# Kernel optimization log

Hardware: AMD Instinct MI355X
Metric: run time of the kernel (lower is better)

The kernel has to match this reference:

```python
import jax, jax.numpy as jnp
import numpy as np

N_NODES = 50000
N_REL = 20
EMB = 64
HID = 128
N_EDGES = 1600000
BATCH = 8192


def _rgcn_layer(x, src, dst, etype, W, root, b):
    # PyG RGCNConv with aggr='mean', no basis decomposition:
    # out[i] = sum_r W_r @ mean_{j in N_r(i)} x[j] + root @ x[i] + b
    # Mean commutes with the linear map, so aggregate x[src] per (dst, rel)
    # first, then apply W_r once per relation.
    n, r = N_NODES, N_REL
    seg = dst * r + etype                                   # [E]
    msg = x[src]                                            # [E, d_in]
    agg = jax.ops.segment_sum(msg, seg, num_segments=n * r)  # [N*R, d_in]
    cnt = jax.ops.segment_sum(jnp.ones(src.shape, x.dtype), seg, num_segments=n * r)
    mean = agg / jnp.maximum(cnt, 1.0)[:, None]
    mean = mean.reshape(n, r, -1)                           # [N, R, d_in]
    return jnp.einsum('nri,rio->no', mean, W) + x @ root + b


def setup_inputs() -> dict:
    key = jax.random.key(0)
    ks = jax.random.split(key, 16)
    edge_index = jax.random.randint(ks[0], (2, N_EDGES), 0, N_NODES, dtype=jnp.int64 if jax.config.jax_enable_x64 else jnp.int32)
    edge_type = jax.random.randint(ks[1], (N_EDGES,), 0, N_REL)
    head_indices = jax.random.randint(ks[2], (BATCH,), 0, N_NODES)
    tail_indices = jax.random.randint(ks[3], (BATCH,), 0, N_NODES)
    relation_types = jax.random.randint(ks[4], (BATCH,), 0, N_REL)

    def xavier(k, shape):
        fan_in, fan_out = shape[-2], shape[-1]
        lim = float(np.sqrt(6.0 / (fan_in + fan_out)))
        return jax.random.uniform(k, shape, jnp.float32, -lim, lim)

    node_emb = xavier(ks[5], (N_NODES, EMB))
    W1 = xavier(ks[6], (N_REL, EMB, HID))
    root1 = xavier(ks[7], (EMB, HID))
    b1 = jnp.zeros((HID,), jnp.float32)
    W2 = xavier(ks[8], (N_REL, HID, HID))
    root2 = xavier(ks[9], (HID, HID))
    b2 = jnp.zeros((HID,), jnp.float32)
    rel_emb = xavier(ks[10], (N_REL, HID))
    return dict(edge_index=edge_index, edge_type=edge_type,
                head_indices=head_indices, tail_indices=tail_indices,
                relation_types=relation_types, node_emb=node_emb,
                W1=W1, root1=root1, b1=b1, W2=W2, root2=root2, b2=b2,
                rel_emb=rel_emb)


def reference(edge_index, edge_type, head_indices, tail_indices, relation_types,
              node_emb, W1, root1, b1, W2, root2, b2, rel_emb):
    src, dst = edge_index[0], edge_index[1]
    # RGCN encoder (eval mode: dropout is identity)
    h = _rgcn_layer(node_emb, src, dst, edge_type, W1, root1, b1)
    h = jax.nn.relu(h)
    h = _rgcn_layer(h, src, dst, edge_type, W2, root2, b2)
    # DistMult decoder
    head = h[head_indices]
    tail = h[tail_indices]
    r = rel_emb[relation_types]
    scores = jnp.sum(head * r * tail, axis=1)               # [B]
    return scores
```

## Files before the change

### kernel.cpp

```cpp
#include <hip/hip_runtime.h>
#include <hip/hip_bf16.h>

#define NNODES 50000
#define NREL   20
#define NSEG   (NNODES * NREL)
#define DEMB   64
#define DHID   128

typedef __attribute__((ext_vector_type(8))) short short8;
typedef __attribute__((ext_vector_type(4))) float f32x4;

__device__ __forceinline__ unsigned short bf16rn(float x) {
    unsigned u = __builtin_bit_cast(unsigned, x);
    unsigned r = u + 0x7FFFu + ((u >> 16) & 1u);
    return (unsigned short)(r >> 16);
}
__device__ __forceinline__ float bf16tof(unsigned short h) {
    return __builtin_bit_cast(float, (unsigned)h << 16);
}


__global__ void hist_kernel(const int* __restrict__ dst, const int* __restrict__ et,
                            int E, int* __restrict__ cnt) {
    for (int e = blockIdx.x * blockDim.x + threadIdx.x; e < E; e += gridDim.x * blockDim.x) {
        atomicAdd(&cnt[dst[e] * NREL + et[e]], 1);
    }
}

__global__ void scan_partial(const int* __restrict__ cnt, int* __restrict__ bsum, int n) {
    __shared__ int s[256];
    int base = blockIdx.x * 1024;
    int t = threadIdx.x;
    int v = 0;
    for (int i = t; i < 1024; i += 256) {
        int idx = base + i;
        v += (idx < n) ? cnt[idx] : 0;
    }
    s[t] = v;
    __syncthreads();
    for (int o = 128; o > 0; o >>= 1) {
        if (t < o) s[t] += s[t + o];
        __syncthreads();
    }
    if (t == 0) bsum[blockIdx.x] = s[0];
}

__global__ void scan_bsums(int* __restrict__ bsum, int nb) {
    __shared__ int s[1024];
    int t = threadIdx.x;
    s[t] = (t < nb) ? bsum[t] : 0;
    __syncthreads();
    for (int o = 1; o < 1024; o <<= 1) {
        int v = (t >= o) ? s[t - o] : 0;
        __syncthreads();
        s[t] += v;
        __syncthreads();
    }
    if (t < nb) bsum[t] = (t == 0) ? 0 : s[t - 1];
}

__global__ void scan_final(const int* __restrict__ cnt, const int* __restrict__ bsum,
                           int* __restrict__ off, int n) {
    __shared__ int s[256];
    int base = blockIdx.x * 1024;
    int t = threadIdx.x;
    int idx = base + t * 4;
    int a0 = (idx + 0 < n) ? cnt[idx + 0] : 0;
    int a1 = (idx + 1 < n) ? cnt[idx + 1] : 0;
    int a2 = (idx + 2 < n) ? cnt[idx + 2] : 0;
    int a3 = (idx + 3 < n) ? cnt[idx + 3] : 0;
    s[t] = a0 + a1 + a2 + a3;
    __syncthreads();
    for (int o = 1; o < 256; o <<= 1) {
        int v = (t >= o) ? s[t - o] : 0;
        __syncthreads();
        s[t] += v;
        __syncthreads();
    }
    int base_ex = ((t == 0) ? 0 : s[t - 1]) + bsum[blockIdx.x];
    if (idx + 0 < n) off[idx + 0] = base_ex;
    if (idx + 1 < n) off[idx + 1] = base_ex + a0;
    if (idx + 2 < n) off[idx + 2] = base_ex + a0 + a1;
    if (idx + 3 < n) off[idx + 3] = base_ex + a0 + a1 + a2;
}

__global__ void place_kernel(const int* __restrict__ src, const int* __restrict__ dst,
                             const int* __restrict__ et, int E,
                             int* __restrict__ off_mut, int* __restrict__ csr_src) {
    for (int e = blockIdx.x * blockDim.x + threadIdx.x; e < E; e += gridDim.x * blockDim.x) {
        int seg = dst[e] * NREL + et[e];
        int p = atomicAdd(&off_mut[seg], 1);
        csr_src[p] = src[e];
    }
}

template <int K>
__global__ void prep_w(const float* __restrict__ W, const float* __restrict__ root,
                       short* __restrict__ Wt) {
    constexpr int KS = K / 32;
    int idx = blockIdx.x * blockDim.x + threadIdx.x;
    int total = (NREL + 1) * 128 * K;
    if (idx >= total) return;
    int r   = idx / (128 * K);
    int rem = idx % (128 * K);
    int c   = rem / K;
    int k   = rem % K;
    float v = (r < NREL) ? W[((size_t)r * K + k) * 128 + c] : root[(size_t)k * 128 + c];
    unsigned short hi = bf16rn(v);
    unsigned short lo = bf16rn(v - bf16tof(hi));
    int s = k >> 5, kk = k & 31;
    size_t base = ((size_t)r * KS + s) * 10240 + (size_t)c * 40 + kk;
    Wt[base]        = (short)hi;
    Wt[base + 5120] = (short)lo;
}


__device__ __forceinline__ void stage20(const short* __restrict__ gsrc,
                                        short* ldst, int t) {
    const int u = t >> 6, lane = t & 63;
    #pragma unroll
    for (int j = 0; j < 3; ++j) {
        int blk = u + j * 8;
        if (blk >= 20) break;
        __builtin_amdgcn_global_load_lds(
            (const __attribute__((address_space(1))) void*)((const char*)gsrc + blk * 1024 + lane * 16),
            (__attribute__((address_space(3))) void*)((char*)ldst + blk * 1024 + lane * 16),
            16, 0, 0);
    }
}

template <int K, bool RELU_IN>
__global__ __launch_bounds__(512, 4) void rgcn_layer_kernel(
    const float* __restrict__ X,
    const short* __restrict__ Wt,
    const float* __restrict__ bias,
    const int* __restrict__ off,
    const int* __restrict__ cnt,
    const int* __restrict__ csr_src,
    float* __restrict__ H,
    int nnodes)
{
    constexpr int NB  = 128;
    constexpr int NQ  = K / 32;
    constexpr int KS  = K / 32;
    constexpr int QSs = 40;
    constexpr int PSq = NB * QSs;

    __shared__ short meanS[2 * PSq];
    __shared__ short Wbuf[10240];

    const int n0 = blockIdx.x * NB;
    const int ry = blockIdx.y;
    const int t  = threadIdx.x;
    const int l  = t & 63;
    const int w  = t >> 6;
    const int rg = w & 3;
    const int cg = w >> 2;
    const int q8 = (l >> 4) * 8;

    const int team  = t >> 3;
    const int lane8 = t & 7;

    f32x4 acc[2][4];
    #pragma unroll
    for (int ct = 0; ct < 4; ++ct) {
        const float b = (ry == 0) ? bias[cg * 64 + ct * 16 + (l & 15)] : 0.0f;
        #pragma unroll
        for (int rt = 0; rt < 2; ++rt) acc[rt][ct] = (f32x4){b, b, b, b};
    }

    const int r0 = ry ? 11 : 0;
    const int r1 = ry ? 21 : 11;

    for (int rr = r0; rr < r1; ++rr) {
        __syncthreads();

        const short* wtRel = Wt + (size_t)rr * KS * 10240;
        stage20(wtRel, Wbuf, t);

        const int nA = n0 + team;
        const int nB = n0 + team + 64;
        float sAx[NQ], sAy[NQ], sAz[NQ], sAw[NQ];
        float sBx[NQ], sBy[NQ], sBz[NQ], sBw[NQ];
        #pragma unroll
        for (int q = 0; q < NQ; ++q) {
            sAx[q] = sAy[q] = sAz[q] = sAw[q] = 0.f;
            sBx[q] = sBy[q] = sBz[q] = sBw[q] = 0.f;
        }

        if (rr < NREL) {
            int cA = 0, oA = 0, cB = 0, oB = 0;
            if (nA < nnodes) { const int sg = nA * NREL + rr; cA = cnt[sg]; oA = off[sg] - cA; }
            if (nB < nnodes) { const int sg = nB * NREL + rr; cB = cnt[sg]; oB = off[sg] - cB; }
            const int jmax = max(cA, cB);
            for (int j = 0; j < jmax; ++j) {
                const bool pa = j < cA, pb = j < cB;
                const int ia = csr_src[pa ? (oA + j) : 0];
                const int ib = csr_src[pb ? (oB + j) : 0];
                const float* pxA = X + (size_t)ia * K;
                const float* pxB = X + (size_t)ib * K;
                float4 vA[NQ], vB[NQ];
                #pragma unroll
                for (int q = 0; q < NQ; ++q) vA[q] = *(const float4*)&pxA[q * 32 + lane8 * 4];
                #pragma unroll
                for (int q = 0; q < NQ; ++q) vB[q] = *(const float4*)&pxB[q * 32 + lane8 * 4];
                if (RELU_IN) {
                    #pragma unroll
                    for (int q = 0; q < NQ; ++q) {
                        vA[q].x = fmaxf(vA[q].x, 0.f); vA[q].y = fmaxf(vA[q].y, 0.f);
                        vA[q].z = fmaxf(vA[q].z, 0.f); vA[q].w = fmaxf(vA[q].w, 0.f);
                        vB[q].x = fmaxf(vB[q].x, 0.f); vB[q].y = fmaxf(vB[q].y, 0.f);
                        vB[q].z = fmaxf(vB[q].z, 0.f); vB[q].w = fmaxf(vB[q].w, 0.f);
                    }
                }
                if (pa) {
                    #pragma unroll
                    for (int q = 0; q < NQ; ++q) {
                        sAx[q] += vA[q].x; sAy[q] += vA[q].y; sAz[q] += vA[q].z; sAw[q] += vA[q].w;
                    }
                }
                if (pb) {
                    #pragma unroll
                    for (int q = 0; q < NQ; ++q) {
                        sBx[q] += vB[q].x; sBy[q] += vB[q].y; sBz[q] += vB[q].z; sBw[q] += vB[q].w;
                    }
                }
            }
            const float invA = 1.0f / (float)max(cA, 1);
            const float invB = 1.0f / (float)max(cB, 1);
            #pragma unroll
            for (int q = 0; q < NQ; ++q) {
                sAx[q] *= invA; sAy[q] *= invA; sAz[q] *= invA; sAw[q] *= invA;
                sBx[q] *= invB; sBy[q] *= invB; sBz[q] *= invB; sBw[q] *= invB;
            }
        } else {
            if (nA < nnodes) {
                const float* xr = X + (size_t)nA * K;
                #pragma unroll
                for (int q = 0; q < NQ; ++q) {
                    float4 v = *(const float4*)&xr[q * 32 + lane8 * 4];
                    if (RELU_IN) { v.x = fmaxf(v.x, 0.f); v.y = fmaxf(v.y, 0.f);
                                   v.z = fmaxf(v.z, 0.f); v.w = fmaxf(v.w, 0.f); }
                    sAx[q] = v.x; sAy[q] = v.y; sAz[q] = v.z; sAw[q] = v.w;
                }
            }
            if (nB < nnodes) {
                const float* xr = X + (size_t)nB * K;
                #pragma unroll
                for (int q = 0; q < NQ; ++q) {
                    float4 v = *(const float4*)&xr[q * 32 + lane8 * 4];
                    if (RELU_IN) { v.x = fmaxf(v.x, 0.f); v.y = fmaxf(v.y, 0.f);
                                   v.z = fmaxf(v.z, 0.f); v.w = fmaxf(v.w, 0.f); }
                    sBx[q] = v.x; sBy[q] = v.y; sBz[q] = v.z; sBw[q] = v.w;
                }
            }
        }

        #pragma unroll
        for (int q = 0; q < KS; ++q) {
            if (q > 0) {
                __syncthreads();
                stage20(wtRel + q * 10240, Wbuf, t);
            }
            {
                const int kb = lane8 * 4;
                {
                    const float vx = sAx[q], vy = sAy[q], vz = sAz[q], vw = sAw[q];
                    const unsigned short hx = bf16rn(vx), hy = bf16rn(vy), hz = bf16rn(vz), hw = bf16rn(vw);
                    short4 hi4, lo4;
                    hi4.x = (short)hx; hi4.y = (short)hy; hi4.z = (short)hz; hi4.w = (short)hw;
                    lo4.x = (short)bf16rn(vx - bf16tof(hx));
                    lo4.y = (short)bf16rn(vy - bf16tof(hy));
                    lo4.z = (short)bf16rn(vz - bf16tof(hz));
                    lo4.w = (short)bf16rn(vw - bf16tof(hw));
                    *(short4*)&meanS[team * QSs + kb]       = hi4;
                    *(short4*)&meanS[PSq + team * QSs + kb] = lo4;
                }
                {
                    const float vx = sBx[q], vy = sBy[q], vz = sBz[q], vw = sBw[q];
                    const unsigned short hx = bf16rn(vx), hy = bf16rn(vy), hz = bf16rn(vz), hw = bf16rn(vw);
                    short4 hi4, lo4;
                    hi4.x = (short)hx; hi4.y = (short)hy; hi4.z = (short)hz; hi4.w = (short)hw;
                    lo4.x = (short)bf16rn(vx - bf16tof(hx));
                    lo4.y = (short)bf16rn(vy - bf16tof(hy));
                    lo4.z = (short)bf16rn(vz - bf16tof(hz));
                    lo4.w = (short)bf16rn(vw - bf16tof(hw));
                    *(short4*)&meanS[(team + 64) * QSs + kb]       = hi4;
                    *(short4*)&meanS[PSq + (team + 64) * QSs + kb] = lo4;
                }
            }
            __syncthreads();

            short8 bhi[4], blo[4];
            #pragma unroll
            for (int ct = 0; ct < 4; ++ct) {
                const int col = cg * 64 + ct * 16 + (l & 15);
                bhi[ct] = *(const short8*)&Wbuf[       col * 40 + q8];
                blo[ct] = *(const short8*)&Wbuf[5120 + col * 40 + q8];
            }

            #pragma unroll
            for (int rt = 0; rt < 2; ++rt) {
                const int row = rg * 32 + rt * 16 + (l & 15);
                const int ka  = row * QSs + q8;
                const short8 a0 = *(const short8*)&meanS[ka];
                const short8 a1 = *(const short8*)&meanS[PSq + ka];
                #pragma unroll
                for (int ct = 0; ct < 4; ++ct) {
                    acc[rt][ct] = __builtin_amdgcn_mfma_f32_16x16x32_bf16(a0, bhi[ct], acc[rt][ct], 0, 0, 0);
                    acc[rt][ct] = __builtin_amdgcn_mfma_f32_16x16x32_bf16(a0, blo[ct], acc[rt][ct], 0, 0, 0);
                    acc[rt][ct] = __builtin_amdgcn_mfma_f32_16x16x32_bf16(a1, bhi[ct], acc[rt][ct], 0, 0, 0);
                }
            }
        }
    }

    #pragma unroll
    for (int rt = 0; rt < 2; ++rt) {
        #pragma unroll
        for (int reg = 0; reg < 4; ++reg) {
            const int node = n0 + rg * 32 + rt * 16 + (l >> 4) * 4 + reg;
            if (node < nnodes) {
                #pragma unroll
                for (int ct = 0; ct < 4; ++ct) {
                    atomicAdd(&H[(size_t)node * 128 + cg * 64 + ct * 16 + (l & 15)],
                              acc[rt][ct][reg]);
                }
            }
        }
    }
}

__global__ void decoder_kernel(const float* __restrict__ H, const float* __restrict__ rel_emb,
                               const int* __restrict__ head, const int* __restrict__ tail,
                               const int* __restrict__ rt, float* __restrict__ out, int B) {
    const int idx  = blockIdx.x * blockDim.x + threadIdx.x;
    const int b    = idx >> 6;
    const int lane = idx & 63;
    if (b >= B) return;
    const float* hp = H + (size_t)head[b] * 128;
    const float* tp = H + (size_t)tail[b] * 128;
    const float* rp = rel_emb + (size_t)rt[b] * 128;
    double s = 0.0;
    #pragma unroll
    for (int c = 0; c < 2; ++c) {
        const int k = lane + c * 64;
        s += (double)hp[k] * (double)rp[k] * (double)tp[k];
    }
    for (int o = 32; o > 0; o >>= 1) s += __shfl_down(s, o);
    if (lane == 0) out[b] = (float)s;
}


extern "C" void kernel_launch(void* const* d_in, const int* in_sizes, int n_in,
                              void* d_out, int out_size, void* d_ws, size_t ws_size,
                              hipStream_t stream) {
    const int*   edge_index = (const int*)d_in[0];
    const int*   edge_type  = (const int*)d_in[1];
    const int*   head       = (const int*)d_in[2];
    const int*   tail       = (const int*)d_in[3];
    const int*   rtyp       = (const int*)d_in[4];
    const float* node_emb   = (const float*)d_in[5];
    const float* W1         = (const float*)d_in[6];
    const float* root1      = (const float*)d_in[7];
    const float* b1         = (const float*)d_in[8];
    const float* W2         = (const float*)d_in[9];
    const float* root2      = (const float*)d_in[10];
    const float* b2         = (const float*)d_in[11];
    const float* rel_emb    = (const float*)d_in[12];
    float* out = (float*)d_out;

    const int E = in_sizes[1];
    const int B = in_sizes[2];
    const int* src = edge_index;
    const int* dst = edge_index + E;

    char* ws = (char*)d_ws;
    size_t o = 0;
    auto carve = [&](size_t bytes) { char* p = ws + o; o += (bytes + 255) & ~size_t(255); return p; };
    int*   off     = (int*)carve(sizeof(int) * NSEG);
    int*   cnt     = (int*)carve(sizeof(int) * NSEG);
    int*   csr_src = (int*)carve(sizeof(int) * (size_t)E);
    int*   bsum    = (int*)carve(sizeof(int) * 1024);
    float* h1      = (float*)carve(sizeof(float) * (size_t)NNODES * DHID);
    float* h2      = (float*)carve(sizeof(float) * (size_t)NNODES * DHID);
    short* Wt1     = (short*)carve(sizeof(short) * (size_t)(NREL + 1) * 2 * 10240);
    short* Wt2     = (short*)carve(sizeof(short) * (size_t)(NREL + 1) * 4 * 10240);
    (void)ws_size;

    const int NCHUNK = (NSEG + 1023) / 1024;

    {
        const int tot1 = (NREL + 1) * 128 * DEMB;
        const int tot2 = (NREL + 1) * 128 * DHID;
        prep_w<DEMB><<<(tot1 + 255) / 256, 256, 0, stream>>>(W1, root1, Wt1);
        prep_w<DHID><<<(tot2 + 255) / 256, 256, 0, stream>>>(W2, root2, Wt2);
    }

    hipMemsetAsync(cnt, 0, sizeof(int) * NSEG, stream);
    hist_kernel<<<2048, 256, 0, stream>>>(dst, edge_type, E, cnt);
    scan_partial<<<NCHUNK, 256, 0, stream>>>(cnt, bsum, NSEG);
    scan_bsums<<<1, 1024, 0, stream>>>(bsum, NCHUNK);
    scan_final<<<NCHUNK, 256, 0, stream>>>(cnt, bsum, off, NSEG);
    place_kernel<<<2048, 256, 0, stream>>>(src, dst, edge_type, E, off, csr_src);

    hipMemsetAsync(h1, 0, sizeof(float) * (size_t)NNODES * DHID, stream);
    hipMemsetAsync(h2, 0, sizeof(float) * (size_t)NNODES * DHID, stream);

    const dim3 LGRID((NNODES + 127) / 128, 2);
    rgcn_layer_kernel<DEMB, false><<<LGRID, 512, 0, stream>>>(node_emb, Wt1, b1,
                                                              off, cnt, csr_src, h1, NNODES);
    rgcn_layer_kernel<DHID, true ><<<LGRID, 512, 0, stream>>>(h1, Wt2, b2,
                                                              off, cnt, csr_src, h2, NNODES);

    decoder_kernel<<<(B * 64 + 255) / 256, 256, 0, stream>>>(h2, rel_emb, head, tail, rtyp, out, B);
}
```

Before: 762.3 us.

## Shrink layer tile to 32 nodes with 256 threads, preload CSR metadata, unroll gather by three

Reworks the fused RGCN layer kernel to process 32 nodes per block with 256 threads (one node per 8-thread team) instead of 128 nodes with 512 threads. Per-block cnt/off values for all relations are preloaded into shared memory, and the neighbour gather loop is unrolled by three to keep more loads in flight. The aim is more blocks and better latency hiding for the irregular gather, and less divergence from pairing two nodes with different degrees. In exchange, each 20 KB weight slice is staged per 32 nodes rather than per 128, quadrupling weight traffic into LDS, and the clamped duplicate loads at the tail of each unrolled iteration are wasted work.

After: 687.1 us. 9.9% less time.

```diff
diff --git a/kernel.cpp b/kernel.cpp
--- a/kernel.cpp
+++ b/kernel.cpp
@@ -119,9 +119,8 @@
                                         short* ldst, int t) {
     const int u = t >> 6, lane = t & 63;
     #pragma unroll
-    for (int j = 0; j < 3; ++j) {
-        int blk = u + j * 8;
-        if (blk >= 20) break;
+    for (int j = 0; j < 5; ++j) {
+        const int blk = u + j * 4;
         __builtin_amdgcn_global_load_lds(
             (const __attribute__((address_space(1))) void*)((const char*)gsrc + blk * 1024 + lane * 16),
             (__attribute__((address_space(3))) void*)((char*)ldst + blk * 1024 + lane * 16),
@@ -130,7 +129,7 @@
 }
 
 template <int K, bool RELU_IN>
-__global__ __launch_bounds__(512, 4) void rgcn_layer_kernel(
+__global__ __launch_bounds__(256, 4) void rgcn_layer_kernel(
     const float* __restrict__ X,
     const short* __restrict__ Wt,
     const float* __restrict__ bias,
@@ -140,31 +139,43 @@
     float* __restrict__ H,
     int nnodes)
 {
-    constexpr int NB  = 128;
+    constexpr int NB  = 32;
     constexpr int NQ  = K / 32;
     constexpr int KS  = K / 32;
-    constexpr int QSs = 40;
+    constexpr int QSs = 56;
     constexpr int PSq = NB * QSs;
 
-    __shared__ short meanS[2 * PSq];
-    __shared__ short Wbuf[10240];
+    __shared__ short          meanS[2 * PSq];
+    __shared__ short          Wbuf[10240];
+    __shared__ unsigned short cntS[NB * NREL];
+    __shared__ int            offS[NB * NREL];
 
     const int n0 = blockIdx.x * NB;
     const int ry = blockIdx.y;
     const int t  = threadIdx.x;
     const int l  = t & 63;
-    const int w  = t >> 6;
-    const int rg = w & 3;
-    const int cg = w >> 2;
+    const int wv = t >> 6;
     const int q8 = (l >> 4) * 8;
 
     const int team  = t >> 3;
     const int lane8 = t & 7;
-
-    f32x4 acc[2][4];
+    const int node  = n0 + team;
+
+    {
+        const int base = n0 * NREL;
+        for (int i = t; i < NB * NREL; i += 256) {
+            const int nn = n0 + i / NREL;
+            int vc = 0, vo = 0;
+            if (nn < nnodes) { vc = cnt[base + i]; vo = off[base + i]; }
+            cntS[i] = (unsigned short)vc;
+            offS[i] = vo;
+        }
+    }
+
+    f32x4 acc[2][2];
     #pragma unroll
-    for (int ct = 0; ct < 4; ++ct) {
-        const float b = (ry == 0) ? bias[cg * 64 + ct * 16 + (l & 15)] : 0.0f;
+    for (int ct = 0; ct < 2; ++ct) {
+        const float b = (ry == 0) ? bias[wv * 32 + ct * 16 + (l & 15)] : 0.0f;
         #pragma unroll
         for (int rt = 0; rt < 2; ++rt) acc[rt][ct] = (f32x4){b, b, b, b};
     }
@@ -178,81 +189,68 @@
         const short* wtRel = Wt + (size_t)rr * KS * 10240;
         stage20(wtRel, Wbuf, t);
 
-        const int nA = n0 + team;
-        const int nB = n0 + team + 64;
-        float sAx[NQ], sAy[NQ], sAz[NQ], sAw[NQ];
-        float sBx[NQ], sBy[NQ], sBz[NQ], sBw[NQ];
+        float sx[NQ], sy[NQ], sz[NQ], sw[NQ];
         #pragma unroll
-        for (int q = 0; q < NQ; ++q) {
-            sAx[q] = sAy[q] = sAz[q] = sAw[q] = 0.f;
-            sBx[q] = sBy[q] = sBz[q] = sBw[q] = 0.f;
-        }
+        for (int q = 0; q < NQ; ++q) { sx[q] = sy[q] = sz[q] = sw[q] = 0.f; }
 
         if (rr < NREL) {
-            int cA = 0, oA = 0, cB = 0, oB = 0;
-            if (nA < nnodes) { const int sg = nA * NREL + rr; cA = cnt[sg]; oA = off[sg] - cA; }
-            if (nB < nnodes) { const int sg = nB * NREL + rr; cB = cnt[sg]; oB = off[sg] - cB; }
-            const int jmax = max(cA, cB);
-            for (int j = 0; j < jmax; ++j) {
-                const bool pa = j < cA, pb = j < cB;
-                const int ia = csr_src[pa ? (oA + j) : 0];
-                const int ib = csr_src[pb ? (oB + j) : 0];
-                const float* pxA = X + (size_t)ia * K;
-                const float* pxB = X + (size_t)ib * K;
-                float4 vA[NQ], vB[NQ];
-                #pragma unroll
-                for (int q = 0; q < NQ; ++q) vA[q] = *(const float4*)&pxA[q * 32 + lane8 * 4];
-                #pragma unroll
-                for (int q = 0; q < NQ; ++q) vB[q] = *(const float4*)&pxB[q * 32 + lane8 * 4];
+            const int c  = cntS[team * NREL + rr];
+            const int s0 = offS[team * NREL + rr] - c;
+            for (int j = 0; j < c; j += 3) {
+                const int e1 = min(j + 1, c - 1);
+                const int e2 = min(j + 2, c - 1);
+                const int i0 = csr_src[s0 + j];
+                const int i1 = csr_src[s0 + e1];
+                const int i2 = csr_src[s0 + e2];
+                const float* p0 = X + (size_t)i0 * K + lane8 * 4;
+                const float* p1 = X + (size_t)i1 * K + lane8 * 4;
+                const float* p2 = X + (size_t)i2 * K + lane8 * 4;
+                float4 v0[NQ], v1[NQ], v2[NQ];
+                #pragma unroll
+                for (int q = 0; q < NQ; ++q) v0[q] = *(const float4*)&p0[q * 32];
+                #pragma unroll
+                for (int q = 0; q < NQ; ++q) v1[q] = *(const float4*)&p1[q * 32];
+                #pragma unroll
+                for (int q = 0; q < NQ; ++q) v2[q] = *(const float4*)&p2[q * 32];
                 if (RELU_IN) {
                     #pragma unroll
                     for (int q = 0; q < NQ; ++q) {
-                        vA[q].x = fmaxf(vA[q].x, 0.f); vA[q].y = fmaxf(vA[q].y, 0.f);
-                        vA[q].z = fmaxf(vA[q].z, 0.f); vA[q].w = fmaxf(vA[q].w, 0.f);
-                        vB[q].x = fmaxf(vB[q].x, 0.f); vB[q].y = fmaxf(vB[q].y, 0.f);
-                        vB[q].z = fmaxf(vB[q].z, 0.f); vB[q].w = fmaxf(vB[q].w, 0.f);
+                        v0[q].x = fmaxf(v0[q].x, 0.f); v0[q].y = fmaxf(v0[q].y, 0.f);
+                        v0[q].z = fmaxf(v0[q].z, 0.f); v0[q].w = fmaxf(v0[q].w, 0.f);
+                        v1[q].x = fmaxf(v1[q].x, 0.f); v1[q].y = fmaxf(v1[q].y, 0.f);
+                        v1[q].z = fmaxf(v1[q].z, 0.f); v1[q].w = fmaxf(v1[q].w, 0.f);
+                        v2[q].x = fmaxf(v2[q].x, 0.f); v2[q].y = fmaxf(v2[q].y, 0.f);
+                        v2[q].z = fmaxf(v2[q].z, 0.f); v2[q].w = fmaxf(v2[q].w, 0.f);
                     }
                 }
-                if (pa) {
+                #pragma unroll
+                for (int q = 0; q < NQ; ++q) {
+                    sx[q] += v0[q].x; sy[q] += v0[q].y; sz[q] += v0[q].z; sw[q] += v0[q].w;
+                }
+                if (j + 1 < c) {
                     #pragma unroll
                     for (int q = 0; q < NQ; ++q) {
-                        sAx[q] += vA[q].x; sAy[q] += vA[q].y; sAz[q] += vA[q].z; sAw[q] += vA[q].w;
+                        sx[q] += v1[q].x; sy[q] += v1[q].y; sz[q] += v1[q].z; sw[q] += v1[q].w;
                     }
                 }
-                if (pb) {
+                if (j + 2 < c) {
                     #pragma unroll
                     for (int q = 0; q < NQ; ++q) {
-                        sBx[q] += vB[q].x; sBy[q] += vB[q].y; sBz[q] += vB[q].z; sBw[q] += vB[q].w;
+                        sx[q] += v2[q].x; sy[q] += v2[q].y; sz[q] += v2[q].z; sw[q] += v2[q].w;
                     }
                 }
             }
-            const float invA = 1.0f / (float)max(cA, 1);
-            const float invB = 1.0f / (float)max(cB, 1);
+            const float inv = 1.0f / (float)max(c, 1);
+            #pragma unroll
+            for (int q = 0; q < NQ; ++q) { sx[q] *= inv; sy[q] *= inv; sz[q] *= inv; sw[q] *= inv; }
+        } else if (node < nnodes) {
+            const float* xr = X + (size_t)node * K + lane8 * 4;
             #pragma unroll
             for (int q = 0; q < NQ; ++q) {
-                sAx[q] *= invA; sAy[q] *= invA; sAz[q] *= invA; sAw[q] *= invA;
-                sBx[q] *= invB; sBy[q] *= invB; sBz[q] *= invB; sBw[q] *= invB;
-            }
-        } else {
-            if (nA < nnodes) {
-                const float* xr = X + (size_t)nA * K;
-                #pragma unroll
-                for (int q = 0; q < NQ; ++q) {
-                    float4 v = *(const float4*)&xr[q * 32 + lane8 * 4];
-                    if (RELU_IN) { v.x = fmaxf(v.x, 0.f); v.y = fmaxf(v.y, 0.f);
-                                   v.z = fmaxf(v.z, 0.f); v.w = fmaxf(v.w, 0.f); }
-                    sAx[q] = v.x; sAy[q] = v.y; sAz[q] = v.z; sAw[q] = v.w;
-                }
-            }
-            if (nB < nnodes) {
-                const float* xr = X + (size_t)nB * K;
-                #pragma unroll
-                for (int q = 0; q < NQ; ++q) {
-                    float4 v = *(const float4*)&xr[q * 32 + lane8 * 4];
-                    if (RELU_IN) { v.x = fmaxf(v.x, 0.f); v.y = fmaxf(v.y, 0.f);
-                                   v.z = fmaxf(v.z, 0.f); v.w = fmaxf(v.w, 0.f); }
-                    sBx[q] = v.x; sBy[q] = v.y; sBz[q] = v.z; sBw[q] = v.w;
-                }
+                float4 v = *(const float4*)&xr[q * 32];
+                if (RELU_IN) { v.x = fmaxf(v.x, 0.f); v.y = fmaxf(v.y, 0.f);
+                               v.z = fmaxf(v.z, 0.f); v.w = fmaxf(v.w, 0.f); }
+                sx[q] = v.x; sy[q] = v.y; sz[q] = v.z; sw[q] = v.w;
             }
         }
 
@@ -263,50 +261,36 @@
                 stage20(wtRel + q * 10240, Wbuf, t);
             }
             {
-                const int kb = lane8 * 4;
-                {
-                    const float vx = sAx[q], vy = sAy[q], vz = sAz[q], vw = sAw[q];
-                    const unsigned short hx = bf16rn(vx), hy = bf16rn(vy), hz = bf16rn(vz), hw = bf16rn(vw);
-                    short4 hi4, lo4;
-                    hi4.x = (short)hx; hi4.y = (short)hy; hi4.z = (short)hz; hi4.w = (short)hw;
-                    lo4.x = (short)bf16rn(vx - bf16tof(hx));
-                    lo4.y = (short)bf16rn(vy - bf16tof(hy));
-                    lo4.z = (short)bf16rn(vz - bf16tof(hz));
-                    lo4.w = (short)bf16rn(vw - bf16tof(hw));
-                    *(short4*)&meanS[team * QSs + kb]       = hi4;
-                    *(short4*)&meanS[PSq + team * QSs + kb] = lo4;
-                }
-                {
-                    const float vx = sBx[q], vy = sBy[q], vz = sBz[q], vw = sBw[q];
-                    const unsigned short hx = bf16rn(vx), hy = bf16rn(vy), hz = bf16rn(vz), hw = bf16rn(vw);
-                    short4 hi4, lo4;
-                    hi4.x = (short)hx; hi4.y = (short)hy; hi4.z = (short)hz; hi4.w = (short)hw;
-                    lo4.x = (short)bf16rn(vx - bf16tof(hx));
-                    lo4.y = (short)bf16rn(vy - bf16tof(hy));
-                    lo4.z = (short)bf16rn(vz - bf16tof(hz));
-                    lo4.w = (short)bf16rn(vw - bf16tof(hw));
-                    *(short4*)&meanS[(team + 64) * QSs + kb]       = hi4;
-                    *(short4*)&meanS[PSq + (team + 64) * QSs + kb] = lo4;
-                }
+                const float vx = sx[q], vy = sy[q], vz = sz[q], vw = sw[q];
+                const unsigned short hx = bf16rn(vx), hy = bf16rn(vy), hz = bf16rn(vz), hw = bf16rn(vw);
+                short4 hi4, lo4;
+                hi4.x = (short)hx; hi4.y = (short)hy; hi4.z = (short)hz; hi4.w = (short)hw;
+                lo4.x = (short)bf16rn(vx - bf16tof(hx));
+                lo4.y = (short)bf16rn(vy - bf16tof(hy));
+                lo4.z = (short)bf16rn(vz - bf16tof(hz));
+                lo4.w = (short)bf16rn(vw - bf16tof(hw));
+                const int kb = team * QSs + lane8 * 4;
+                *(short4*)&meanS[kb]       = hi4;
+                *(short4*)&meanS[PSq + kb] = lo4;
             }
             __syncthreads();
 
-            short8 bhi[4], blo[4];
+            short8 bhi[2], blo[2];
             #pragma unroll
-            for (int ct = 0; ct < 4; ++ct) {
-                const int col = cg * 64 + ct * 16 + (l & 15);
+            for (int ct = 0; ct < 2; ++ct) {
+                const int col = wv * 32 + ct * 16 + (l & 15);
                 bhi[ct] = *(const short8*)&Wbuf[       col * 40 + q8];
                 blo[ct] = *(const short8*)&Wbuf[5120 + col * 40 + q8];
             }
 
             #pragma unroll
             for (int rt = 0; rt < 2; ++rt) {
-                const int row = rg * 32 + rt * 16 + (l & 15);
+                const int row = rt * 16 + (l & 15);
                 const int ka  = row * QSs + q8;
                 const short8 a0 = *(const short8*)&meanS[ka];
                 const short8 a1 = *(const short8*)&meanS[PSq + ka];
                 #pragma unroll
-                for (int ct = 0; ct < 4; ++ct) {
+                for (int ct = 0; ct < 2; ++ct) {
                     acc[rt][ct] = __builtin_amdgcn_mfma_f32_16x16x32_bf16(a0, bhi[ct], acc[rt][ct], 0, 0, 0);
                     acc[rt][ct] = __builtin_amdgcn_mfma_f32_16x16x32_bf16(a0, blo[ct], acc[rt][ct], 0, 0, 0);
                     acc[rt][ct] = __builtin_amdgcn_mfma_f32_16x16x32_bf16(a1, bhi[ct], acc[rt][ct], 0, 0, 0);
@@ -319,11 +303,11 @@
     for (int rt = 0; rt < 2; ++rt) {
         #pragma unroll
         for (int reg = 0; reg < 4; ++reg) {
-            const int node = n0 + rg * 32 + rt * 16 + (l >> 4) * 4 + reg;
-            if (node < nnodes) {
-                #pragma unroll
-                for (int ct = 0; ct < 4; ++ct) {
-                    atomicAdd(&H[(size_t)node * 128 + cg * 64 + ct * 16 + (l & 15)],
+            const int n = n0 + rt * 16 + (l >> 4) * 4 + reg;
+            if (n < nnodes) {
+                #pragma unroll
+                for (int ct = 0; ct < 2; ++ct) {
+                    atomicAdd(&H[(size_t)n * 128 + wv * 32 + ct * 16 + (l & 15)],
                               acc[rt][ct][reg]);
                 }
             }
@@ -407,10 +391,10 @@
     hipMemsetAsync(h1, 0, sizeof(float) * (size_t)NNODES * DHID, stream);
     hipMemsetAsync(h2, 0, sizeof(float) * (size_t)NNODES * DHID, stream);
 
-    const dim3 LGRID((NNODES + 127) / 128, 2);
-    rgcn_layer_kernel<DEMB, false><<<LGRID, 512, 0, stream>>>(node_emb, Wt1, b1,
+    const dim3 LGRID((NNODES + 31) / 32, 2);
+    rgcn_layer_kernel<DEMB, false><<<LGRID, 256, 0, stream>>>(node_emb, Wt1, b1,
                                                               off, cnt, csr_src, h1, NNODES);
-    rgcn_layer_kernel<DHID, true ><<<LGRID, 512, 0, stream>>>(h1, Wt2, b2,
+    rgcn_layer_kernel<DHID, true ><<<LGRID, 256, 0, stream>>>(h1, Wt2, b2,
                                                               off, cnt, csr_src, h2, NNODES);
 
     decoder_kernel<<<(B * 64 + 255) / 256, 256, 0, stream>>>(h2, rel_emb, head, tail, rtyp, out, B);
```
